# Performance work log

Measured on AMD Instinct MI355X. Metric: run time of the kernel, lower is better.

The kernel has to match this reference:

```python
import jax, jax.numpy as jnp
import numpy as np

EPS = 1e-5

def _act_quant(x):
    # per-token int8 absmax quantization with STE passthrough
    s = 127.0 / jnp.clip(jnp.max(jnp.abs(x), axis=-1, keepdims=True), EPS, None)
    xq = jnp.clip(jnp.round(x * s), -128.0, 127.0) / s
    return x + jax.lax.stop_gradient(xq - x)

def _weight_quant(w):
    # ternary {-1,0,1} abs-mean quantization with STE passthrough
    s = 1.0 / jnp.clip(jnp.mean(jnp.abs(w)), EPS, None)
    wq = jnp.clip(jnp.round(w * s), -1.0, 1.0) / s
    return w + jax.lax.stop_gradient(wq - w)

def bitlinear(x, w, b=None):
    y = _act_quant(x) @ _weight_quant(w).T
    return y if b is None else y + b

def setup_inputs() -> dict:
    key = jax.random.key(0)
    ks = jax.random.split(key, 6)
    B, T, C = 64, 256, 1024
    std = 1.0 / np.sqrt(C)
    return {
        "x": jax.random.normal(ks[0], (B, T, C), dtype=jnp.float32),
        "Wq": jax.random.normal(ks[1], (C, C), dtype=jnp.float32) * std,
        "Wk": jax.random.normal(ks[2], (C, C), dtype=jnp.float32) * std,
        "Wv": jax.random.normal(ks[3], (C, C), dtype=jnp.float32) * std,
        "Wp": jax.random.normal(ks[4], (C, C), dtype=jnp.float32) * std,
        "bp": jnp.zeros((C,), dtype=jnp.float32),
        "n_head": 16,
    }

def reference(x, Wq, Wk, Wv, Wp, bp, n_head):
    B, T, C = x.shape
    hd = C // n_head
    def heads(t):  # [B,T,C] -> [B,H,T,hd]
        return t.reshape(B, T, n_head, hd).transpose(0, 2, 1, 3)
    q = heads(bitlinear(x, Wq))
    k = heads(bitlinear(x, Wk))
    v = heads(bitlinear(x, Wv))
    attn = jnp.einsum("bhqd,bhkd->bhqk", q, k) * (1.0 / np.sqrt(hd))
    causal = jnp.tril(jnp.ones((T, T), dtype=bool))
    attn = jnp.where(causal, attn, -jnp.inf)
    attn = jax.nn.softmax(attn, axis=-1)
    y = jnp.einsum("bhqk,bhkd->bhqd", attn, v)
    y = y.transpose(0, 2, 1, 3).reshape(B, T, C)
    return bitlinear(y, Wp, bp)
```

## Files before the change

### kernel.cpp

```cpp
#include <hip/hip_runtime.h>
#include <math.h>

#define AS1 __attribute__((address_space(1)))
#define AS3 __attribute__((address_space(3)))

typedef unsigned short u16;
typedef signed char i8;
typedef short bf16x8 __attribute__((ext_vector_type(8)));
typedef float f32x4 __attribute__((ext_vector_type(4)));
typedef int i32x4 __attribute__((ext_vector_type(4)));

static constexpr int BB = 64, T = 256, C = 1024, H = 16, HD = 64;
static constexpr int M = BB * T;
static constexpr float EPSF = 1e-5f;

static constexpr size_t W8_OFF   = 0;
static constexpr size_t XQ8_OFF  = 4ull  << 20;
static constexpr size_t RSX_OFF  = 20ull << 20;
static constexpr size_t RSY_OFF  = (20ull << 20) + (64 << 10);
static constexpr size_t WSUM_OFF = (20ull << 20) + (128 << 10);
static constexpr size_t WPART_OFF= WSUM_OFF + 64;
static constexpr size_t QB_OFF   = 21ull << 20;
static constexpr size_t KB_OFF   = 53ull << 20;
static constexpr size_t VT_OFF   = 85ull << 20;

__device__ __forceinline__ u16 f2bf_rne(float f) {
    unsigned x = __float_as_uint(f);
    unsigned r = x + 0x7FFF + ((x >> 16) & 1);
    return (u16)(r >> 16);
}

__global__ __launch_bounds__(256) void wsum1_kernel(const float* __restrict__ Wq,
    const float* __restrict__ Wk, const float* __restrict__ Wv,
    const float* __restrict__ Wp, double* __restrict__ wpart)
{
    const int mat = blockIdx.x >> 6;
    const float* W = (mat == 0) ? Wq : (mat == 1) ? Wk : (mat == 2) ? Wv : Wp;
    const int t = threadIdx.x;
    const int base = (blockIdx.x & 63) * 256 + t;
    double s = 0.0;
    for (int i = 0; i < 64; ++i) s += (double)fabsf(W[base + (i << 14)]);
    #pragma unroll
    for (int off = 32; off >= 1; off >>= 1) s += __shfl_down(s, off);
    __shared__ double red[4];
    if ((t & 63) == 0) red[t >> 6] = s;
    __syncthreads();
    if (t == 0) wpart[blockIdx.x] = red[0] + red[1] + red[2] + red[3];
}

__global__ __launch_bounds__(256) void wsum2_kernel(const double* __restrict__ wpart,
                                                    double* __restrict__ wsum)
{
    const int t = threadIdx.x;
    double s = wpart[t];
    #pragma unroll
    for (int off = 32; off >= 1; off >>= 1) s += __shfl_down(s, off);
    if ((t & 63) == 0) wsum[t >> 6] = s;
}

__global__ __launch_bounds__(256) void wquant_kernel(const float* __restrict__ Wq,
    const float* __restrict__ Wk, const float* __restrict__ Wv,
    const float* __restrict__ Wp, const double* __restrict__ wsum,
    i8* __restrict__ w8)
{
    const int mat = blockIdx.x >> 10;
    const float* W = (mat == 0) ? Wq : (mat == 1) ? Wk : (mat == 2) ? Wv : Wp;
    const float mean = (float)(wsum[mat] * (1.0 / 1048576.0));
    const float s = 1.0f / fmaxf(mean, EPSF);
    const int idx = (blockIdx.x & 1023) * 256 + threadIdx.x;
    float4 w = ((const float4*)W)[idx];
    char4 o;
    o.x = (i8)(int)fminf(fmaxf(rintf(w.x * s), -1.f), 1.f);
    o.y = (i8)(int)fminf(fmaxf(rintf(w.y * s), -1.f), 1.f);
    o.z = (i8)(int)fminf(fmaxf(rintf(w.z * s), -1.f), 1.f);
    o.w = (i8)(int)fminf(fmaxf(rintf(w.w * s), -1.f), 1.f);
    ((char4*)(w8 + (size_t)mat * 1048576))[idx] = o;
}

__global__ __launch_bounds__(256) void actquant_kernel(const float* __restrict__ x,
    i8* __restrict__ xq, float* __restrict__ rs)
{
    const int row = blockIdx.x;
    const int t = threadIdx.x;
    float4 v = ((const float4*)(x + (size_t)row * C))[t];
    float m = fmaxf(fmaxf(fabsf(v.x), fabsf(v.y)), fmaxf(fabsf(v.z), fabsf(v.w)));
    #pragma unroll
    for (int off = 32; off >= 1; off >>= 1) m = fmaxf(m, __shfl_down(m, off));
    __shared__ float red[4];
    if ((t & 63) == 0) red[t >> 6] = m;
    __syncthreads();
    float mm = fmaxf(fmaxf(red[0], red[1]), fmaxf(red[2], red[3]));
    mm = fmaxf(mm, EPSF);
    const float s = 127.0f / mm;
    if (t == 0) rs[row] = mm / 127.0f;
    char4 o;
    o.x = (i8)(int)fminf(fmaxf(rintf(v.x * s), -128.f), 127.f);
    o.y = (i8)(int)fminf(fmaxf(rintf(v.y * s), -128.f), 127.f);
    o.z = (i8)(int)fminf(fmaxf(rintf(v.z * s), -128.f), 127.f);
    o.w = (i8)(int)fminf(fmaxf(rintf(v.w * s), -128.f), 127.f);
    ((char4*)(xq + (size_t)row * C))[t] = o;
}

template<bool QKV, int NNB>
__global__ __launch_bounds__(512, 2) void gemm_kernel(const i8* __restrict__ A,
    const i8* __restrict__ w8, const float* __restrict__ rs_row,
    const double* __restrict__ wsum, u16* __restrict__ qb, u16* __restrict__ kb,
    u16* __restrict__ vt, float* __restrict__ outp, const float* __restrict__ bias)
{
    constexpr int K = 1024, N = 1024;
    constexpr int NT = 16;
    __shared__ __align__(16) i8 Asm[4][256 * 64];
    __shared__ __align__(16) i8 Bsm[4][256 * 64];

    const int t = threadIdx.x;

    const int nwg = NNB * 64;
    const int wg = (int)blockIdx.x;
    const int swz = (wg & 7) * (nwg >> 3) + (wg >> 3);
    const int mb = swz / NNB, nb = swz % NNB;
    const int m0 = mb * 256;
    const int mat = QKV ? (nb >> 2) : 3;
    const int n0m = QKV ? ((nb & 3) * 256) : (nb * 256);
    const i8* Bw = w8 + (size_t)mat * 1048576;

    const int lane = t & 63, wv = t >> 6;
    const int wm = wv >> 2, wn = wv & 3;
    const int mr = lane & 15, quad = lane >> 4;

    const int g1 = t, g2 = t + 512;
    const int L1 = (g1 * 16) ^ (((g1 >> 3) & 7) << 4);
    const int L2 = (g2 * 16) ^ (((g2 >> 3) & 7) << 4);
    const i8* a1 = A  + (size_t)(m0  + (L1 >> 6)) * K + (L1 & 63);
    const i8* a2 = A  + (size_t)(m0  + (L2 >> 6)) * K + (L2 & 63);
    const i8* b1 = Bw + (size_t)(n0m + (L1 >> 6)) * K + (L1 & 63);
    const i8* b2 = Bw + (size_t)(n0m + (L2 >> 6)) * K + (L2 & 63);

    const int vvs = (mr >> 1) & 7;
    int aoff[8], boff[4];
    #pragma unroll
    for (int m = 0; m < 8; ++m)
        aoff[m] = ((wm * 128 + m * 16 + mr) * 64 + quad * 16) ^ (vvs << 4);
    #pragma unroll
    for (int n = 0; n < 4; ++n)
        boff[n] = ((wn * 64 + n * 16 + mr) * 64 + quad * 16) ^ (vvs << 4);

    i32x4 acc[8][4];
    #pragma unroll
    for (int m = 0; m < 8; ++m)
        #pragma unroll
        for (int n = 0; n < 4; ++n) acc[m][n] = (i32x4){0, 0, 0, 0};

    #pragma unroll
    for (int p = 0; p < 2; ++p) {
        const int k0 = p * 64;
        __builtin_amdgcn_global_load_lds((const AS1 void*)(a1 + k0), (AS3 void*)&Asm[p][g1 * 16], 16, 0, 0);
        __builtin_amdgcn_global_load_lds((const AS1 void*)(a2 + k0), (AS3 void*)&Asm[p][g2 * 16], 16, 0, 0);
        __builtin_amdgcn_global_load_lds((const AS1 void*)(b1 + k0), (AS3 void*)&Bsm[p][g1 * 16], 16, 0, 0);
        __builtin_amdgcn_global_load_lds((const AS1 void*)(b2 + k0), (AS3 void*)&Bsm[p][g2 * 16], 16, 0, 0);
    }
    asm volatile("s_waitcnt vmcnt(4)" ::: "memory");
    __builtin_amdgcn_s_barrier();

    for (int tt = 0; tt < NT; ++tt) {
        const i8* Ac = Asm[tt & 3];
        const i8* Bc = Bsm[tt & 3];
        i8* An = Asm[(tt + 2) & 3];
        i8* Bn = Bsm[(tt + 2) & 3];
        const int kn = (tt + 2) * 64;
        const bool pf = (tt < NT - 2);

        if (pf) {
            __builtin_amdgcn_global_load_lds((const AS1 void*)(a1 + kn), (AS3 void*)&An[g1 * 16], 16, 0, 0);
            __builtin_amdgcn_global_load_lds((const AS1 void*)(a2 + kn), (AS3 void*)&An[g2 * 16], 16, 0, 0);
        }
        i32x4 af[8];
        #pragma unroll
        for (int m = 0; m < 8; ++m) af[m] = *(const i32x4*)&Ac[aoff[m]];
        i32x4 bf0 = *(const i32x4*)&Bc[boff[0]];
        i32x4 bf1 = *(const i32x4*)&Bc[boff[1]];
        __builtin_amdgcn_s_barrier();
        asm volatile("s_waitcnt lgkmcnt(0)" ::: "memory");
        __builtin_amdgcn_s_setprio(1);
        #pragma unroll
        for (int m = 0; m < 8; ++m) {
            acc[m][0] = __builtin_amdgcn_mfma_i32_16x16x64_i8(af[m], bf0, acc[m][0], 0, 0, 0);
            acc[m][1] = __builtin_amdgcn_mfma_i32_16x16x64_i8(af[m], bf1, acc[m][1], 0, 0, 0);
        }
        __builtin_amdgcn_s_setprio(0);
        __builtin_amdgcn_s_barrier();

        if (pf) {
            __builtin_amdgcn_global_load_lds((const AS1 void*)(b1 + kn), (AS3 void*)&Bn[g1 * 16], 16, 0, 0);
            __builtin_amdgcn_global_load_lds((const AS1 void*)(b2 + kn), (AS3 void*)&Bn[g2 * 16], 16, 0, 0);
        }
        i32x4 bf2 = *(const i32x4*)&Bc[boff[2]];
        i32x4 bf3 = *(const i32x4*)&Bc[boff[3]];
        __builtin_amdgcn_s_barrier();
        asm volatile("s_waitcnt lgkmcnt(0)" ::: "memory");
        __builtin_amdgcn_s_setprio(1);
        #pragma unroll
        for (int m = 0; m < 8; ++m) {
            acc[m][2] = __builtin_amdgcn_mfma_i32_16x16x64_i8(af[m], bf2, acc[m][2], 0, 0, 0);
            acc[m][3] = __builtin_amdgcn_mfma_i32_16x16x64_i8(af[m], bf3, acc[m][3], 0, 0, 0);
        }
        __builtin_amdgcn_s_setprio(0);
        if (tt < NT - 2) {
            asm volatile("s_waitcnt vmcnt(4)" ::: "memory");
        } else if (tt < NT - 1) {
            asm volatile("s_waitcnt vmcnt(0)" ::: "memory");
        }
        __builtin_amdgcn_s_barrier();
    }

    float wsc = fmaxf((float)(wsum[mat] * (1.0 / 1048576.0)), EPSF);
    if (QKV && mat == 0) wsc *= 0.125f;

    if (QKV && mat == 2) {
        #pragma unroll
        for (int m = 0; m < 8; ++m) {
            const int gr0 = m0 + wm * 128 + m * 16 + quad * 4;
            const int bbi = gr0 >> 8, tl = gr0 & 255;
            const float4 rs4 = *(const float4*)(rs_row + gr0);
            #pragma unroll
            for (int n = 0; n < 4; ++n) {
                const int gcol = n0m + wn * 64 + n * 16 + mr;
                ushort4 o;
                o.x = f2bf_rne((float)acc[m][n][0] * rs4.x * wsc);
                o.y = f2bf_rne((float)acc[m][n][1] * rs4.y * wsc);
                o.z = f2bf_rne((float)acc[m][n][2] * rs4.z * wsc);
                o.w = f2bf_rne((float)acc[m][n][3] * rs4.w * wsc);
                *(ushort4*)(vt + (size_t)(bbi * 1024 + gcol) * 256 + tl) = o;
            }
        }
        return;
    }

    u16* ob = QKV ? ((mat == 0) ? qb : kb) : nullptr;
    #pragma unroll
    for (int m = 0; m < 8; ++m) {
        const int gr0 = m0 + wm * 128 + m * 16 + quad * 4;
        #pragma unroll
        for (int r = 0; r < 4; ++r) {
            const int grow = gr0 + r;
            const float sc = rs_row[grow] * wsc;
            #pragma unroll
            for (int n = 0; n < 4; ++n) {
                const int gcol = n0m + wn * 64 + n * 16 + mr;
                const float val = (float)acc[m][n][r] * sc;
                if (QKV) {
                    ob[(size_t)grow * N + gcol] = f2bf_rne(val);
                } else {
                    outp[(size_t)grow * N + gcol] = val + bias[gcol];
                }
            }
        }
    }
}

__global__ __launch_bounds__(256) void attn_kernel(const u16* __restrict__ qb,
    const u16* __restrict__ kb, const u16* __restrict__ vt, float* __restrict__ y)
{
    const int t = threadIdx.x;
    const int qt = 3 - (int)(blockIdx.x >> 10);
    const int bh = blockIdx.x & 1023;
    const int b = bh >> 4, h = bh & 15;
    const int w = t >> 6, lane = t & 63;
    const int cl = lane & 15, quad = lane >> 4;
    const size_t gb = (size_t)(b * T) * 1024 + h * 64;
    const u16* vtb = vt + (size_t)(b * 1024 + h * 64) * 256;

    const int qrow = qt * 64 + w * 16;
    const int jtiles = (qrow >> 4) + 1;

    const u16* qrp = qb + gb + (size_t)(qrow + cl) * 1024 + quad * 8;
    bf16x8 qf0 = *(const bf16x8*)qrp;
    bf16x8 qf1 = *(const bf16x8*)(qrp + 32);

    f32x4 Sp[16];
    #pragma unroll
    for (int i = 0; i < 16; ++i) Sp[i] = (f32x4){0.f, 0.f, 0.f, 0.f};

    const u16* krp = kb + gb + (size_t)cl * 1024 + quad * 8;
    #pragma unroll
    for (int jt = 0; jt < 16; ++jt) {
        if (jt < jtiles) {
            const u16* kp = krp + (size_t)(jt * 16) * 1024;
            bf16x8 kf0 = *(const bf16x8*)kp;
            bf16x8 kf1 = *(const bf16x8*)(kp + 32);
            Sp[jt] = __builtin_amdgcn_mfma_f32_16x16x32_bf16(kf0, qf0, Sp[jt], 0, 0, 0);
            Sp[jt] = __builtin_amdgcn_mfma_f32_16x16x32_bf16(kf1, qf1, Sp[jt], 0, 0, 0);
            if (jt == jtiles - 1) {
                #pragma unroll
                for (int r = 0; r < 4; ++r)
                    if (quad * 4 + r > cl) Sp[jt][r] = -INFINITY;
            }
        }
    }

    float mx = -INFINITY;
    #pragma unroll
    for (int jt = 0; jt < 16; ++jt) if (jt < jtiles) {
        #pragma unroll
        for (int r = 0; r < 4; ++r) mx = fmaxf(mx, Sp[jt][r]);
    }
    mx = fmaxf(mx, __shfl_xor(mx, 16));
    mx = fmaxf(mx, __shfl_xor(mx, 32));
    float l = 0.f;
    #pragma unroll
    for (int jt = 0; jt < 16; ++jt) if (jt < jtiles) {
        #pragma unroll
        for (int r = 0; r < 4; ++r) {
            float p = __expf(Sp[jt][r] - mx);
            Sp[jt][r] = p;
            l += p;
        }
    }
    l += __shfl_xor(l, 16);
    l += __shfl_xor(l, 32);

    f32x4 O[4];
    #pragma unroll
    for (int i = 0; i < 4; ++i) O[i] = (f32x4){0.f, 0.f, 0.f, 0.f};

    const int s01 = ((quad & 1) << 5) + cl;
    const bool lo = quad < 2;
    #pragma unroll
    for (int jc = 0; jc < 8; ++jc) {
        if (jc * 2 < jtiles) {
            int pk[2][2];
            #pragma unroll
            for (int s = 0; s < 2; ++s) {
                const f32x4 v = Sp[jc * 2 + s];
                pk[s][0] = (int)((unsigned)f2bf_rne(v[0]) | ((unsigned)f2bf_rne(v[1]) << 16));
                pk[s][1] = (int)((unsigned)f2bf_rne(v[2]) | ((unsigned)f2bf_rne(v[3]) << 16));
            }
            int a0 = __shfl(pk[0][0], s01),      a1 = __shfl(pk[0][1], s01);
            int a2 = __shfl(pk[0][0], s01 + 16), a3 = __shfl(pk[0][1], s01 + 16);
            int b0 = __shfl(pk[1][0], s01),      b1 = __shfl(pk[1][1], s01);
            int b2 = __shfl(pk[1][0], s01 + 16), b3 = __shfl(pk[1][1], s01 + 16);
            union { int i[4]; bf16x8 v; } af;
            af.i[0] = lo ? a0 : b0;
            af.i[1] = lo ? a1 : b1;
            af.i[2] = lo ? a2 : b2;
            af.i[3] = lo ? a3 : b3;
            const u16* vp = vtb + (size_t)cl * 256 + jc * 32 + quad * 8;
            #pragma unroll
            for (int dt = 0; dt < 4; ++dt) {
                bf16x8 vf = *(const bf16x8*)(vp + (size_t)dt * 16 * 256);
                O[dt] = __builtin_amdgcn_mfma_f32_16x16x32_bf16(af.v, vf, O[dt], 0, 0, 0);
            }
        }
    }

    float inv[4];
    #pragma unroll
    for (int r = 0; r < 4; ++r) inv[r] = 1.0f / __shfl(l, quad * 4 + r);
    #pragma unroll
    for (int dt = 0; dt < 4; ++dt)
        #pragma unroll
        for (int r = 0; r < 4; ++r)
            y[gb + (size_t)(qrow + quad * 4 + r) * 1024 + dt * 16 + cl] = O[dt][r] * inv[r];
}

extern "C" void kernel_launch(void* const* d_in, const int* in_sizes, int n_in,
                              void* d_out, int out_size, void* d_ws, size_t ws_size,
                              hipStream_t stream) {
    (void)in_sizes; (void)n_in; (void)out_size; (void)ws_size;
    const float* x  = (const float*)d_in[0];
    const float* Wq = (const float*)d_in[1];
    const float* Wk = (const float*)d_in[2];
    const float* Wv = (const float*)d_in[3];
    const float* Wp = (const float*)d_in[4];
    const float* bp = (const float*)d_in[5];
    float* out = (float*)d_out;
    char* ws = (char*)d_ws;

    i8*     w8   = (i8*)(ws + W8_OFF);
    i8*     xq8  = (i8*)(ws + XQ8_OFF);
    float*  rsx  = (float*)(ws + RSX_OFF);
    float*  rsy  = (float*)(ws + RSY_OFF);
    double* wsum = (double*)(ws + WSUM_OFF);
    double* wpart= (double*)(ws + WPART_OFF);
    u16*    qb   = (u16*)(ws + QB_OFF);
    u16*    kb   = (u16*)(ws + KB_OFF);
    u16*    vt   = (u16*)(ws + VT_OFF);

    wsum1_kernel<<<256, 256, 0, stream>>>(Wq, Wk, Wv, Wp, wpart);
    wsum2_kernel<<<1, 256, 0, stream>>>(wpart, wsum);
    wquant_kernel<<<4096, 256, 0, stream>>>(Wq, Wk, Wv, Wp, wsum, w8);
    actquant_kernel<<<M, 256, 0, stream>>>(x, xq8, rsx);

    gemm_kernel<true, 12><<<768, 512, 0, stream>>>(xq8, w8, rsx, wsum, qb, kb, vt, nullptr, nullptr);

    attn_kernel<<<4 * 1024, 256, 0, stream>>>(qb, kb, vt, out);

    actquant_kernel<<<M, 256, 0, stream>>>(out, xq8, rsy);
    gemm_kernel<false, 4><<<256, 512, 0, stream>>>(xq8, w8, rsy, wsum, nullptr, nullptr, nullptr, out, bp);
}
```

Baseline: 322.0 us.

## Restructure int8 GEMM main loop and prefetch K/V in attention kernel

The int8 GEMM loop now issues all four global-to-LDS prefetches up front, loads every A/B fragment at once, and runs all 32 MFMAs in one block. This removes two of the three barriers per K-step, and sched_barrier fences keep the compiler from reordering across iterations. The attention kernel software-pipelines K and V fragment loads with double-buffered registers so global loads overlap the MFMAs. It also remaps block indices so neighbouring blocks share batch/head groups across q-tiles, which may improve cache locality. The cost is higher register pressure, which may lower occupancy.

```diff
diff --git a/kernel.cpp b/kernel.cpp
--- a/kernel.cpp
+++ b/kernel.cpp
@@ -160,6 +160,7 @@
     }
     asm volatile("s_waitcnt vmcnt(4)" ::: "memory");
     __builtin_amdgcn_s_barrier();
+    __builtin_amdgcn_sched_barrier(0);
 
     for (int tt = 0; tt < NT; ++tt) {
         const i8* Ac = Asm[tt & 3];
@@ -167,49 +168,35 @@
         i8* An = Asm[(tt + 2) & 3];
         i8* Bn = Bsm[(tt + 2) & 3];
         const int kn = (tt + 2) * 64;
-        const bool pf = (tt < NT - 2);
-
-        if (pf) {
+
+        if (tt < NT - 2) {
             __builtin_amdgcn_global_load_lds((const AS1 void*)(a1 + kn), (AS3 void*)&An[g1 * 16], 16, 0, 0);
             __builtin_amdgcn_global_load_lds((const AS1 void*)(a2 + kn), (AS3 void*)&An[g2 * 16], 16, 0, 0);
-        }
-        i32x4 af[8];
-        #pragma unroll
-        for (int m = 0; m < 8; ++m) af[m] = *(const i32x4*)&Ac[aoff[m]];
-        i32x4 bf0 = *(const i32x4*)&Bc[boff[0]];
-        i32x4 bf1 = *(const i32x4*)&Bc[boff[1]];
-        __builtin_amdgcn_s_barrier();
-        asm volatile("s_waitcnt lgkmcnt(0)" ::: "memory");
-        __builtin_amdgcn_s_setprio(1);
-        #pragma unroll
-        for (int m = 0; m < 8; ++m) {
-            acc[m][0] = __builtin_amdgcn_mfma_i32_16x16x64_i8(af[m], bf0, acc[m][0], 0, 0, 0);
-            acc[m][1] = __builtin_amdgcn_mfma_i32_16x16x64_i8(af[m], bf1, acc[m][1], 0, 0, 0);
-        }
-        __builtin_amdgcn_s_setprio(0);
-        __builtin_amdgcn_s_barrier();
-
-        if (pf) {
             __builtin_amdgcn_global_load_lds((const AS1 void*)(b1 + kn), (AS3 void*)&Bn[g1 * 16], 16, 0, 0);
             __builtin_amdgcn_global_load_lds((const AS1 void*)(b2 + kn), (AS3 void*)&Bn[g2 * 16], 16, 0, 0);
         }
-        i32x4 bf2 = *(const i32x4*)&Bc[boff[2]];
-        i32x4 bf3 = *(const i32x4*)&Bc[boff[3]];
-        __builtin_amdgcn_s_barrier();
-        asm volatile("s_waitcnt lgkmcnt(0)" ::: "memory");
+
+        i32x4 af[8], bf[4];
+        #pragma unroll
+        for (int m = 0; m < 8; ++m) af[m] = *(const i32x4*)&Ac[aoff[m]];
+        #pragma unroll
+        for (int n = 0; n < 4; ++n) bf[n] = *(const i32x4*)&Bc[boff[n]];
+
         __builtin_amdgcn_s_setprio(1);
         #pragma unroll
-        for (int m = 0; m < 8; ++m) {
-            acc[m][2] = __builtin_amdgcn_mfma_i32_16x16x64_i8(af[m], bf2, acc[m][2], 0, 0, 0);
-            acc[m][3] = __builtin_amdgcn_mfma_i32_16x16x64_i8(af[m], bf3, acc[m][3], 0, 0, 0);
-        }
+        for (int m = 0; m < 8; ++m)
+            #pragma unroll
+            for (int n = 0; n < 4; ++n)
+                acc[m][n] = __builtin_amdgcn_mfma_i32_16x16x64_i8(af[m], bf[n], acc[m][n], 0, 0, 0);
         __builtin_amdgcn_s_setprio(0);
+
         if (tt < NT - 2) {
             asm volatile("s_waitcnt vmcnt(4)" ::: "memory");
         } else if (tt < NT - 1) {
             asm volatile("s_waitcnt vmcnt(0)" ::: "memory");
         }
         __builtin_amdgcn_s_barrier();
+        __builtin_amdgcn_sched_barrier(0);
     }
 
     float wsc = fmaxf((float)(wsum[mat] * (1.0 / 1048576.0)), EPSF);
@@ -261,8 +248,9 @@
     const u16* __restrict__ kb, const u16* __restrict__ vt, float* __restrict__ y)
 {
     const int t = threadIdx.x;
-    const int qt = 3 - (int)(blockIdx.x >> 10);
-    const int bh = blockIdx.x & 1023;
+    const int i = (int)blockIdx.x;
+    const int qt = 3 - ((i >> 3) & 3);
+    const int bh = ((i >> 5) << 3) | (i & 7);
     const int b = bh >> 4, h = bh & 15;
     const int w = t >> 6, lane = t & 63;
     const int cl = lane & 15, quad = lane >> 4;
@@ -278,21 +266,44 @@
 
     f32x4 Sp[16];
     #pragma unroll
-    for (int i = 0; i < 16; ++i) Sp[i] = (f32x4){0.f, 0.f, 0.f, 0.f};
+    for (int i2 = 0; i2 < 16; ++i2) Sp[i2] = (f32x4){0.f, 0.f, 0.f, 0.f};
 
     const u16* krp = kb + gb + (size_t)cl * 1024 + quad * 8;
-    #pragma unroll
-    for (int jt = 0; jt < 16; ++jt) {
-        if (jt < jtiles) {
-            const u16* kp = krp + (size_t)(jt * 16) * 1024;
-            bf16x8 kf0 = *(const bf16x8*)kp;
-            bf16x8 kf1 = *(const bf16x8*)(kp + 32);
-            Sp[jt] = __builtin_amdgcn_mfma_f32_16x16x32_bf16(kf0, qf0, Sp[jt], 0, 0, 0);
-            Sp[jt] = __builtin_amdgcn_mfma_f32_16x16x32_bf16(kf1, qf1, Sp[jt], 0, 0, 0);
-            if (jt == jtiles - 1) {
-                #pragma unroll
-                for (int r = 0; r < 4; ++r)
-                    if (quad * 4 + r > cl) Sp[jt][r] = -INFINITY;
+    bf16x8 kA[8], kB[8];
+    #pragma unroll
+    for (int s = 0; s < 4; ++s) {
+        if (s < jtiles) {
+            const u16* kp = krp + (size_t)(s * 16) * 1024;
+            kA[2 * s]     = *(const bf16x8*)kp;
+            kA[2 * s + 1] = *(const bf16x8*)(kp + 32);
+        }
+    }
+    #pragma unroll
+    for (int ch = 0; ch < 4; ++ch) {
+        if (ch * 4 < jtiles) {
+            #pragma unroll
+            for (int s = 0; s < 4; ++s) {
+                const int jn = ch * 4 + 4 + s;
+                if (jn < jtiles) {
+                    const u16* kp = krp + (size_t)(jn * 16) * 1024;
+                    if (ch & 1) { kA[2 * s] = *(const bf16x8*)kp; kA[2 * s + 1] = *(const bf16x8*)(kp + 32); }
+                    else        { kB[2 * s] = *(const bf16x8*)kp; kB[2 * s + 1] = *(const bf16x8*)(kp + 32); }
+                }
+            }
+            #pragma unroll
+            for (int s = 0; s < 4; ++s) {
+                const int jt = ch * 4 + s;
+                if (jt < jtiles) {
+                    const bf16x8 k0 = (ch & 1) ? kB[2 * s]     : kA[2 * s];
+                    const bf16x8 k1 = (ch & 1) ? kB[2 * s + 1] : kA[2 * s + 1];
+                    Sp[jt] = __builtin_amdgcn_mfma_f32_16x16x32_bf16(k0, qf0, Sp[jt], 0, 0, 0);
+                    Sp[jt] = __builtin_amdgcn_mfma_f32_16x16x32_bf16(k1, qf1, Sp[jt], 0, 0, 0);
+                    if (jt == jtiles - 1) {
+                        #pragma unroll
+                        for (int r = 0; r < 4; ++r)
+                            if (quad * 4 + r > cl) Sp[jt][r] = -INFINITY;
+                    }
+                }
             }
         }
     }
@@ -320,13 +331,37 @@
 
     f32x4 O[4];
     #pragma unroll
-    for (int i = 0; i < 4; ++i) O[i] = (f32x4){0.f, 0.f, 0.f, 0.f};
+    for (int i2 = 0; i2 < 4; ++i2) O[i2] = (f32x4){0.f, 0.f, 0.f, 0.f};
+
+    const u16* vpb = vtb + (size_t)cl * 256 + quad * 8;
+    bf16x8 vA0, vA1, vA2, vA3, vB0, vB1, vB2, vB3;
+    {
+        const u16* vp = vpb;
+        vA0 = *(const bf16x8*)vp;
+        vA1 = *(const bf16x8*)(vp + 4096);
+        vA2 = *(const bf16x8*)(vp + 8192);
+        vA3 = *(const bf16x8*)(vp + 12288);
+    }
 
     const int s01 = ((quad & 1) << 5) + cl;
     const bool lo = quad < 2;
     #pragma unroll
     for (int jc = 0; jc < 8; ++jc) {
         if (jc * 2 < jtiles) {
+            if ((jc + 1) * 2 < jtiles) {
+                const u16* vp = vpb + (jc + 1) * 32;
+                if (jc & 1) {
+                    vA0 = *(const bf16x8*)vp;
+                    vA1 = *(const bf16x8*)(vp + 4096);
+                    vA2 = *(const bf16x8*)(vp + 8192);
+                    vA3 = *(const bf16x8*)(vp + 12288);
+                } else {
+                    vB0 = *(const bf16x8*)vp;
+                    vB1 = *(const bf16x8*)(vp + 4096);
+                    vB2 = *(const bf16x8*)(vp + 8192);
+                    vB3 = *(const bf16x8*)(vp + 12288);
+                }
+            }
             int pk[2][2];
             #pragma unroll
             for (int s = 0; s < 2; ++s) {
@@ -343,12 +378,14 @@
             af.i[1] = lo ? a1 : b1;
             af.i[2] = lo ? a2 : b2;
             af.i[3] = lo ? a3 : b3;
-            const u16* vp = vtb + (size_t)cl * 256 + jc * 32 + quad * 8;
-            #pragma unroll
-            for (int dt = 0; dt < 4; ++dt) {
-                bf16x8 vf = *(const bf16x8*)(vp + (size_t)dt * 16 * 256);
-                O[dt] = __builtin_amdgcn_mfma_f32_16x16x32_bf16(af.v, vf, O[dt], 0, 0, 0);
-            }
+            const bf16x8 vf0 = (jc & 1) ? vB0 : vA0;
+            const bf16x8 vf1 = (jc & 1) ? vB1 : vA1;
+            const bf16x8 vf2 = (jc & 1) ? vB2 : vA2;
+            const bf16x8 vf3 = (jc & 1) ? vB3 : vA3;
+            O[0] = __builtin_amdgcn_mfma_f32_16x16x32_bf16(af.v, vf0, O[0], 0, 0, 0);
+            O[1] = __builtin_amdgcn_mfma_f32_16x16x32_bf16(af.v, vf1, O[1], 0, 0, 0);
+            O[2] = __builtin_amdgcn_mfma_f32_16x16x32_bf16(af.v, vf2, O[2], 0, 0, 0);
+            O[3] = __builtin_amdgcn_mfma_f32_16x16x32_bf16(af.v, vf3, O[3], 0, 0, 0);
         }
     }
 
```

After: 349.0 us. 1.08x slower.
